# Kernel optimization log

Measured on AMD Instinct MI355X. Metric: run time of the kernel, lower is better.

Reference implementation:

```python
import jax, jax.numpy as jnp
import numpy as np

N, E, G = 50000, 800000, 64
NODE_IN, EDGE_DIM = 128, 16
H1, C1 = 4, 16            # layer1: 4 heads, 16 ch -> concat 64
H2, C2 = 1, 64            # layer2: 1 head, 64 ch, no concat
OUT = 64


def setup_inputs() -> dict:
    key = jax.random.key(0)
    ks = jax.random.split(key, 20)
    s = 0.05
    inp = {
        "x": jax.random.normal(ks[0], (N, NODE_IN), jnp.float32),
        "edge_index": jax.random.randint(ks[1], (2, E), 0, N, jnp.int32),
        "edge_attr": jax.random.normal(ks[2], (E, EDGE_DIM), jnp.float32),
        "batch": jnp.sort(jax.random.randint(ks[3], (N,), 0, G, jnp.int32)),
        # layer 1 params
        "W1": jax.random.normal(ks[4], (NODE_IN, H1 * C1), jnp.float32) * s,
        "as1": jax.random.normal(ks[5], (H1, C1), jnp.float32) * s,
        "ad1": jax.random.normal(ks[6], (H1, C1), jnp.float32) * s,
        "We1": jax.random.normal(ks[7], (EDGE_DIM, H1 * C1), jnp.float32) * s,
        "ae1": jax.random.normal(ks[8], (H1, C1), jnp.float32) * s,
        "b1": jnp.zeros((H1 * C1,), jnp.float32),
        # layer 2 params
        "W2": jax.random.normal(ks[9], (H1 * C1, H2 * C2), jnp.float32) * s,
        "as2": jax.random.normal(ks[10], (H2, C2), jnp.float32) * s,
        "ad2": jax.random.normal(ks[11], (H2, C2), jnp.float32) * s,
        "We2": jax.random.normal(ks[12], (EDGE_DIM, H2 * C2), jnp.float32) * s,
        "ae2": jax.random.normal(ks[13], (H2, C2), jnp.float32) * s,
        "b2": jnp.zeros((C2,), jnp.float32),
        # final projection
        "Pw": jax.random.normal(ks[14], (OUT, OUT), jnp.float32) * s,
        "Pb": jnp.zeros((OUT,), jnp.float32),
    }
    return inp


def _gat(x, src, dst, edge_attr, W, a_s, a_d, We, a_e, b, heads, ch, concat):
    """PyG GATConv: shared lin, edge features, self-loops with mean fill,
    LeakyReLU(0.2), segment softmax over dst, sum aggregation."""
    n = x.shape[0]
    h = (x @ W).reshape(n, heads, ch)                    # [N,H,C]
    al_s = jnp.einsum("nhc,hc->nh", h, a_s)              # [N,H]
    al_d = jnp.einsum("nhc,hc->nh", h, a_d)
    # add self-loops; loop edge_attr = mean of incoming edge attrs (fill='mean')
    deg = jax.ops.segment_sum(jnp.ones((src.shape[0],), x.dtype), dst, n)
    loop_attr = jax.ops.segment_sum(edge_attr, dst, n) / jnp.maximum(deg, 1.0)[:, None]
    ar = jnp.arange(n, dtype=src.dtype)
    s_idx = jnp.concatenate([src, ar])
    d_idx = jnp.concatenate([dst, ar])
    ea = jnp.concatenate([edge_attr, loop_attr], axis=0)
    al_e = jnp.einsum("ehc,hc->eh", (ea @ We).reshape(-1, heads, ch), a_e)
    alpha = jax.nn.leaky_relu(al_s[s_idx] + al_d[d_idx] + al_e, 0.2)  # [E',H]
    # segment softmax over incoming edges of each dst node
    amax = jax.ops.segment_max(alpha, d_idx, num_segments=n)
    ex = jnp.exp(alpha - amax[d_idx])
    denom = jax.ops.segment_sum(ex, d_idx, num_segments=n)
    att = ex / denom[d_idx]                              # safe: self-loops guarantee denom>0
    msg = h[s_idx] * att[..., None]                      # [E',H,C]
    out = jax.ops.segment_sum(msg.reshape(-1, heads * ch), d_idx, num_segments=n)
    out = out if concat else out.reshape(n, heads, ch).mean(axis=1)
    return out + b


def reference(x, edge_index, edge_attr, batch,
              W1, as1, ad1, We1, ae1, b1,
              W2, as2, ad2, We2, ae2, b2, Pw, Pb):
    src, dst = edge_index[0], edge_index[1]
    h = jax.nn.elu(_gat(x, src, dst, edge_attr, W1, as1, ad1, We1, ae1, b1, H1, C1, True))
    h = _gat(h, src, dst, edge_attr, W2, as2, ad2, We2, ae2, b2, H2, C2, False)
    # global mean pool over graphs
    cnt = jax.ops.segment_sum(jnp.ones((N,), h.dtype), batch, num_segments=G)
    pooled = jax.ops.segment_sum(h, batch, num_segments=G) / jnp.maximum(cnt, 1.0)[:, None]
    return pooled @ Pw + Pb
```

## Files before the change

kernel.cpp:

```cpp
#include <hip/hip_runtime.h>

#define LRELU(a) ((a) > 0.f ? (a) : 0.2f * (a))

__device__ __forceinline__ int blockScanIncl256(int v, int* wl) {
  int t = threadIdx.x, lane = t & 63, w = t >> 6;
  int x = v;
#pragma unroll
  for (int o = 1; o < 64; o <<= 1) {
    int tmp = __shfl_up(x, (unsigned)o, 64);
    if (lane >= o) x += tmp;
  }
  if (lane == 63) wl[w] = x;
  __syncthreads();
  if (t == 0) {
    int s = 0;
#pragma unroll
    for (int j = 0; j < 4; ++j) { int tv = wl[j]; wl[j] = s; s += tv; }
  }
  __syncthreads();
  return x + wl[w];
}

__global__ __launch_bounds__(256) void k_deg(const int* __restrict__ dst,
                                             int* __restrict__ deg, int E) {
  int e = blockIdx.x * 256 + threadIdx.x;
  if (e < E) atomicAdd(&deg[dst[e]], 1);
}

__global__ __launch_bounds__(256) void k_chunksum(const int* __restrict__ deg,
                                                  int* __restrict__ bsum, int n) {
  __shared__ int wl[4];
  int i = blockIdx.x * 256 + threadIdx.x;
  int v = (i < n) ? deg[i] : 0;
#pragma unroll
  for (int o = 1; o < 64; o <<= 1) v += __shfl_xor(v, o, 64);
  int lane = threadIdx.x & 63, w = threadIdx.x >> 6;
  if (lane == 0) wl[w] = v;
  __syncthreads();
  if (threadIdx.x == 0) bsum[blockIdx.x] = wl[0] + wl[1] + wl[2] + wl[3];
}

__global__ __launch_bounds__(256) void k_bscan(int* __restrict__ bsum, int nb,
                                               int* __restrict__ csr_off, int n) {
  __shared__ int wl[4];
  int t = threadIdx.x;
  int v = (t < nb) ? bsum[t] : 0;
  int incl = blockScanIncl256(v, wl);
  if (t < nb) bsum[t] = incl - v;
  if (t == 255) csr_off[n] = incl;
}

__global__ __launch_bounds__(256) void k_chunkscan(const int* __restrict__ deg,
                                                   const int* __restrict__ bsum,
                                                   int* __restrict__ csr_off,
                                                   int* __restrict__ fill, int n) {
  __shared__ int wl[4];
  int i = blockIdx.x * 256 + threadIdx.x;
  int v = (i < n) ? deg[i] : 0;
  int incl = blockScanIncl256(v, wl);
  int o = bsum[blockIdx.x] + incl - v;
  if (i < n) { csr_off[i] = o; fill[i] = o; }
}

template <int K, int HH>
__device__ __forceinline__ void gemm_body(const float* __restrict__ X,
                                          const float* __restrict__ W,
                                          const float* __restrict__ a_s,
                                          const float* __restrict__ a_d,
                                          float* __restrict__ H,
                                          float* __restrict__ als,
                                          float* __restrict__ ald,
                                          int n, int bid) {
  constexpr int KC = 32;
  __shared__ float Xs[64][KC + 4];
  __shared__ float Ws[KC][64 + 4];
  int t = threadIdx.x;
  int b0 = bid * 64;
  int tx = t & 15, ty = t >> 4;
  float acc[4][4] = {};
  for (int kc = 0; kc < K; kc += KC) {
    if (kc) __syncthreads();
    {
      int i = t * 8;
      int node = i >> 5, k = i & 31;
      int r = b0 + node;
      float4 v0 = make_float4(0.f, 0.f, 0.f, 0.f), v1 = v0;
      if (r < n) {
        const float* src = X + (size_t)r * K + kc + k;
        v0 = *(const float4*)src;
        v1 = *(const float4*)(src + 4);
      }
      *(float4*)&Xs[node][k] = v0;
      *(float4*)&Xs[node][k + 4] = v1;
    }
    {
      int i = t * 8;
      int kk = i >> 6, c = i & 63;
      const float* src = W + (size_t)(kc + kk) * 64 + c;
      *(float4*)&Ws[kk][c] = *(const float4*)src;
      *(float4*)&Ws[kk][c + 4] = *(const float4*)(src + 4);
    }
    __syncthreads();
#pragma unroll
    for (int k4 = 0; k4 < KC; k4 += 4) {
      float wvf[4][4];
#pragma unroll
      for (int j = 0; j < 4; ++j)
        *(float4*)&wvf[j][0] = *(const float4*)&Ws[k4 + j][tx * 4];
#pragma unroll
      for (int i = 0; i < 4; ++i) {
        float xvf[4];
        *(float4*)&xvf[0] = *(const float4*)&Xs[ty * 4 + i][k4];
#pragma unroll
        for (int kk = 0; kk < 4; ++kk)
#pragma unroll
          for (int j = 0; j < 4; ++j)
            acc[i][j] = fmaf(xvf[kk], wvf[kk][j], acc[i][j]);
      }
    }
  }
#pragma unroll
  for (int i = 0; i < 4; ++i) {
    int node = b0 + ty * 4 + i;
    if (node < n)
      *(float4*)&H[(size_t)node * 64 + tx * 4] =
          make_float4(acc[i][0], acc[i][1], acc[i][2], acc[i][3]);
  }
  constexpr int C = 64 / HH;
  constexpr int GL = C / 4;
  float asv[4], adv[4];
#pragma unroll
  for (int j = 0; j < 4; ++j) { asv[j] = a_s[tx * 4 + j]; adv[j] = a_d[tx * 4 + j]; }
#pragma unroll
  for (int i = 0; i < 4; ++i) {
    float ps = 0.f, pd = 0.f;
#pragma unroll
    for (int j = 0; j < 4; ++j) {
      ps = fmaf(acc[i][j], asv[j], ps);
      pd = fmaf(acc[i][j], adv[j], pd);
    }
#pragma unroll
    for (int o = 1; o < GL; o <<= 1) {
      ps += __shfl_xor(ps, o, 64);
      pd += __shfl_xor(pd, o, 64);
    }
    int node = b0 + ty * 4 + i;
    if (node < n && (tx & (GL - 1)) == 0) {
      int head = tx / GL;
      als[(size_t)node * HH + head] = ps;
      ald[(size_t)node * HH + head] = pd;
    }
  }
}

__global__ __launch_bounds__(256) void k_gemm2(const float* __restrict__ X,
                                               const float* __restrict__ W,
                                               const float* __restrict__ a_s,
                                               const float* __restrict__ a_d,
                                               float* __restrict__ H,
                                               float* __restrict__ als,
                                               float* __restrict__ ald, int n) {
  gemm_body<64, 1>(X, W, a_s, a_d, H, als, ald, n, blockIdx.x);
}

__global__ __launch_bounds__(256) void k_gs(const float* __restrict__ X,
                                            const float* __restrict__ W,
                                            const float* __restrict__ a_s,
                                            const float* __restrict__ a_d,
                                            float* __restrict__ H,
                                            float* __restrict__ als,
                                            float* __restrict__ ald, int n,
                                            int gemmBlocks,
                                            const int* __restrict__ dst,
                                            const int* __restrict__ src,
                                            int* __restrict__ fill,
                                            int2* __restrict__ pack, int E) {
  if ((int)blockIdx.x < gemmBlocks) {
    gemm_body<128, 4>(X, W, a_s, a_d, H, als, ald, n, blockIdx.x);
  } else {
    int base = (blockIdx.x - gemmBlocks) * 512 + threadIdx.x;
    int e0 = base, e1 = base + 256;
    int d0 = 0, d1 = 0;
    if (e0 < E) d0 = dst[e0];
    if (e1 < E) d1 = dst[e1];
    if (e0 < E) {
      int p = atomicAdd(&fill[d0], 1);
      pack[p] = make_int2(e0, src[e0]);
    }
    if (e1 < E) {
      int p = atomicAdd(&fill[d1], 1);
      pack[p] = make_int2(e1, src[e1]);
    }
  }
}

__global__ __launch_bounds__(256) void k_csrlog(
    const int* __restrict__ csr_off, const int2* __restrict__ pack,
    const float* __restrict__ edge_attr,
    const float* __restrict__ We1, const float* __restrict__ ae1,
    const float* __restrict__ We2, const float* __restrict__ ae2,
    const float* __restrict__ als1, const float* __restrict__ ald1,
    float* __restrict__ elog1, float* __restrict__ selfl1,
    float* __restrict__ ed2csr, float* __restrict__ loopdot2, int n) {
  __shared__ float wa1s[64];
  __shared__ float wa2s[16];
  int t = threadIdx.x;
  if (t < 64) {
    int k = t >> 2, hh = t & 3;
    float s = 0.f;
#pragma unroll
    for (int c = 0; c < 16; ++c) s = fmaf(We1[k * 64 + hh * 16 + c], ae1[hh * 16 + c], s);
    wa1s[t] = s;
  } else if (t < 80) {
    int k = t - 64;
    float s = 0.f;
#pragma unroll
    for (int c = 0; c < 64; ++c) s = fmaf(We2[k * 64 + c], ae2[c], s);
    wa2s[k] = s;
  }
  __syncthreads();
  int g = t >> 4, lane16 = t & 15;
  int node = blockIdx.x * 16 + g;
  if (node >= n) return;
  int s0 = csr_off[node], s1 = csr_off[node + 1];
  float4 adv = *(const float4*)(ald1 + (size_t)node * 4);
  float4 sum1 = make_float4(0.f, 0.f, 0.f, 0.f);
  float sum2 = 0.f;
  for (int i = s0 + lane16; i < s1; i += 16) {
    int2 p = pack[i];
    const float4* ea = (const float4*)(edge_attr + (size_t)p.x * 16);
    float ev[16];
    *(float4*)&ev[0]  = ea[0];
    *(float4*)&ev[4]  = ea[1];
    *(float4*)&ev[8]  = ea[2];
    *(float4*)&ev[12] = ea[3];
    float d0 = 0.f, d1 = 0.f, d2 = 0.f, d3 = 0.f, q = 0.f;
#pragma unroll
    for (int k = 0; k < 16; ++k) {
      float4 w1 = *(const float4*)&wa1s[k * 4];
      d0 = fmaf(ev[k], w1.x, d0);
      d1 = fmaf(ev[k], w1.y, d1);
      d2 = fmaf(ev[k], w1.z, d2);
      d3 = fmaf(ev[k], w1.w, d3);
      q  = fmaf(ev[k], wa2s[k], q);
    }
    sum1.x += d0; sum1.y += d1; sum1.z += d2; sum1.w += d3; sum2 += q;
    float4 asv = *(const float4*)(als1 + (size_t)p.y * 4);
    float l0 = asv.x + adv.x + d0;
    float l1 = asv.y + adv.y + d1;
    float l2 = asv.z + adv.z + d2;
    float l3 = asv.w + adv.w + d3;
    *(float4*)&elog1[(size_t)i * 4] =
        make_float4(LRELU(l0), LRELU(l1), LRELU(l2), LRELU(l3));
    ed2csr[i] = q;
  }
#pragma unroll
  for (int o = 1; o < 16; o <<= 1) {
    sum1.x += __shfl_xor(sum1.x, o, 64);
    sum1.y += __shfl_xor(sum1.y, o, 64);
    sum1.z += __shfl_xor(sum1.z, o, 64);
    sum1.w += __shfl_xor(sum1.w, o, 64);
    sum2   += __shfl_xor(sum2,   o, 64);
  }
  if (lane16 == 0) {
    float cd = fmaxf((float)(s1 - s0), 1.f);
    float4 asn = *(const float4*)(als1 + (size_t)node * 4);
    float l0 = asn.x + adv.x + sum1.x / cd;
    float l1 = asn.y + adv.y + sum1.y / cd;
    float l2 = asn.z + adv.z + sum1.z / cd;
    float l3 = asn.w + adv.w + sum1.w / cd;
    *(float4*)&selfl1[(size_t)node * 4] =
        make_float4(LRELU(l0), LRELU(l1), LRELU(l2), LRELU(l3));
    loopdot2[node] = sum2 / cd;
  }
}

__global__ __launch_bounds__(256) void k_agg1(const int* __restrict__ csr_off,
                                              const int2* __restrict__ pack,
                                              const float* __restrict__ elog,
                                              const float* __restrict__ selfl,
                                              const float* __restrict__ h1,
                                              const float* __restrict__ b1,
                                              float* __restrict__ out1, int n) {
  int t = threadIdx.x, w = t >> 6, lane = t & 63;
  int node = blockIdx.x * 4 + w;
  if (node >= n) return;
  int s0 = csr_off[node], s1 = csr_off[node + 1];
  int nit = s1 - s0;
  int h4 = lane & 3;
  float sl4 = selfl[node * 4 + h4];
  float m = sl4;
  for (int i = s0 + (lane >> 2); i < s1; i += 16)
    m = fmaxf(m, elog[(size_t)i * 4 + h4]);
#pragma unroll
  for (int o = 4; o < 64; o <<= 1) m = fmaxf(m, __shfl_xor(m, o, 64));
  float den = ((lane >> 2) == 0) ? __expf(sl4 - m) : 0.f;
  for (int i = s0 + (lane >> 2); i < s1; i += 16)
    den += __expf(elog[(size_t)i * 4 + h4] - m);
#pragma unroll
  for (int o = 4; o < 64; o <<= 1) den += __shfl_xor(den, o, 64);
  int head = lane >> 4;
  float m_ch = __shfl(m, head, 64);
  float rd_ch = 1.f / __shfl(den, head, 64);
  float sl_ch = __shfl(sl4, head, 64);
  float acc = __expf(sl_ch - m_ch) * h1[(size_t)node * 64 + lane];
  if (nit > 0) {
    int nb = (nit + 7) >> 3;
    int laneE = lane & 7, laneB = (lane >> 2) & 7, laneH = lane & 3;
    int sv; float ev;
    float bufA[8], bufB[8];
    {
      int i1 = min(s0 + laneE, s1 - 1);
      sv = pack[i1].y;
      int i2 = min(s0 + laneB, s1 - 1);
      ev = elog[(size_t)i2 * 4 + laneH];
    }
#pragma unroll
    for (int j = 0; j < 8; ++j)
      bufA[j] = h1[(size_t)__shfl(sv, j, 64) * 64 + lane];
    for (int b = 0; b < nb; ++b) {
      int svN = 0; float evN = 0.f;
      bool pf = (b + 1 < nb);
      if (pf) {
        int base = s0 + (b + 1) * 8;
        int i1 = min(base + laneE, s1 - 1);
        svN = pack[i1].y;
        int i2 = min(base + laneB, s1 - 1);
        evN = elog[(size_t)i2 * 4 + laneH];
#pragma unroll
        for (int j = 0; j < 8; ++j)
          bufB[j] = h1[(size_t)__shfl(svN, j, 64) * 64 + lane];
      }
      int rem = nit - b * 8;
#pragma unroll
      for (int j = 0; j < 8; ++j) {
        float aj = __shfl(ev, j * 4 + head, 64);
        float ex = (j < rem) ? __expf(aj - m_ch) : 0.f;
        acc = fmaf(ex, bufA[j], acc);
      }
      if (pf) {
#pragma unroll
        for (int j = 0; j < 8; ++j) bufA[j] = bufB[j];
        sv = svN; ev = evN;
      }
    }
  }
  float r = acc * rd_ch + b1[lane];
  out1[(size_t)node * 64 + lane] = r > 0.f ? r : expm1f(r);
}

__global__ __launch_bounds__(256) void k_l2log(const int* __restrict__ csr_off,
                                               const int2* __restrict__ pack,
                                               const float* __restrict__ eadot2,
                                               const float* __restrict__ loopdot2,
                                               const float* __restrict__ als2,
                                               const float* __restrict__ ald2,
                                               float* __restrict__ elog2,
                                               float* __restrict__ selfl2, int n) {
  int t = threadIdx.x, w = t >> 6, lane = t & 63;
  int node = blockIdx.x * 4 + w;
  if (node >= n) return;
  float adv = ald2[node];
  if (lane == 0) {
    float lg = als2[node] + adv + loopdot2[node];
    selfl2[node] = LRELU(lg);
  }
  int s0 = csr_off[node], s1 = csr_off[node + 1];
  for (int i = s0 + lane; i < s1; i += 64) {
    int s = pack[i].y;
    float lg = als2[s] + adv + eadot2[i];
    elog2[i] = LRELU(lg);
  }
}

__global__ __launch_bounds__(256) void k_agg2(const int* __restrict__ csr_off,
                                              const int2* __restrict__ pack,
                                              const float* __restrict__ elog,
                                              const float* __restrict__ selfl,
                                              const float* __restrict__ h2,
                                              const float* __restrict__ b2,
                                              float* __restrict__ out2, int n) {
  int t = threadIdx.x, w = t >> 6, lane = t & 63;
  int node = blockIdx.x * 4 + w;
  if (node >= n) return;
  int s0 = csr_off[node], s1 = csr_off[node + 1];
  int nit = s1 - s0;
  float sl = selfl[node];
  float m = sl;
  for (int i = s0 + lane; i < s1; i += 64) m = fmaxf(m, elog[i]);
#pragma unroll
  for (int o = 1; o < 64; o <<= 1) m = fmaxf(m, __shfl_xor(m, o, 64));
  float den = (lane == 0) ? __expf(sl - m) : 0.f;
  for (int i = s0 + lane; i < s1; i += 64) den += __expf(elog[i] - m);
#pragma unroll
  for (int o = 1; o < 64; o <<= 1) den += __shfl_xor(den, o, 64);
  float rd = 1.f / den;
  float acc = __expf(sl - m) * h2[(size_t)node * 64 + lane];
  if (nit > 0) {
    int nb = (nit + 7) >> 3;
    int laneE = lane & 7;
    int sv; float ev;
    {
      int i1 = min(s0 + laneE, s1 - 1);
      sv = pack[i1].y;
      ev = elog[i1];
    }
    float bufA[8], bufB[8];
#pragma unroll
    for (int j = 0; j < 8; ++j)
      bufA[j] = h2[(size_t)__shfl(sv, j, 64) * 64 + lane];
    for (int b = 0; b < nb; ++b) {
      int svN = 0; float evN = 0.f;
      bool pf = (b + 1 < nb);
      if (pf) {
        int i1 = min(s0 + (b + 1) * 8 + laneE, s1 - 1);
        svN = pack[i1].y;
        evN = elog[i1];
#pragma unroll
        for (int j = 0; j < 8; ++j)
          bufB[j] = h2[(size_t)__shfl(svN, j, 64) * 64 + lane];
      }
      int rem = nit - b * 8;
#pragma unroll
      for (int j = 0; j < 8; ++j) {
        float aj = __shfl(ev, j, 64);
        float ex = (j < rem) ? __expf(aj - m) : 0.f;
        acc = fmaf(ex, bufA[j], acc);
      }
      if (pf) {
#pragma unroll
        for (int j = 0; j < 8; ++j) bufA[j] = bufB[j];
        sv = svN; ev = evN;
      }
    }
  }
  out2[(size_t)node * 64 + lane] = acc * rd + b2[lane];
}

__global__ __launch_bounds__(256) void k_pool(const float* __restrict__ out2,
                                              const int* __restrict__ batch,
                                              float* __restrict__ pooled,
                                              float* __restrict__ cnt, int n) {
  int wgl = blockIdx.x * 4 + (threadIdx.x >> 6);
  int lane = threadIdx.x & 63;
  int i0 = wgl * 64;
  if (i0 >= n) return;
  int i1 = min(i0 + 64, n);
  int cur = -1;
  float acc = 0.f, c = 0.f;
  for (int i = i0; i < i1; ++i) {
    int g = batch[i];
    if (g != cur) {
      if (cur >= 0) {
        atomicAdd(&pooled[cur * 64 + lane], acc);
        if (lane == 0) atomicAdd(&cnt[cur], c);
      }
      cur = g; acc = 0.f; c = 0.f;
    }
    acc += out2[(size_t)i * 64 + lane];
    c += 1.f;
  }
  if (cur >= 0) {
    atomicAdd(&pooled[cur * 64 + lane], acc);
    if (lane == 0) atomicAdd(&cnt[cur], c);
  }
}

__global__ __launch_bounds__(64) void k_final(const float* __restrict__ pooled,
                                              const float* __restrict__ cnt,
                                              const float* __restrict__ Pw,
                                              const float* __restrict__ Pb,
                                              float* __restrict__ out) {
  __shared__ float m[64];
  int g = blockIdx.x, o = threadIdx.x;
  m[o] = pooled[g * 64 + o] / fmaxf(cnt[g], 1.f);
  __syncthreads();
  float s = Pb[o];
#pragma unroll
  for (int c = 0; c < 64; ++c) s = fmaf(m[c], Pw[c * 64 + o], s);
  out[g * 64 + o] = s;
}

extern "C" void kernel_launch(void* const* d_in, const int* in_sizes, int n_in,
                              void* d_out, int out_size, void* d_ws, size_t ws_size,
                              hipStream_t stream) {
  const float* x         = (const float*)d_in[0];
  const int*   edge_index= (const int*)d_in[1];
  const float* edge_attr = (const float*)d_in[2];
  const int*   batch     = (const int*)d_in[3];
  const float* W1  = (const float*)d_in[4];
  const float* as1 = (const float*)d_in[5];
  const float* ad1 = (const float*)d_in[6];
  const float* We1 = (const float*)d_in[7];
  const float* ae1 = (const float*)d_in[8];
  const float* b1  = (const float*)d_in[9];
  const float* W2  = (const float*)d_in[10];
  const float* as2 = (const float*)d_in[11];
  const float* ad2 = (const float*)d_in[12];
  const float* We2 = (const float*)d_in[13];
  const float* ae2 = (const float*)d_in[14];
  const float* b2  = (const float*)d_in[15];
  const float* Pw  = (const float*)d_in[16];
  const float* Pb  = (const float*)d_in[17];

  const int N = in_sizes[0] / 128;
  const int E = in_sizes[1] / 2;
  const int G = out_size / 64;
  const int* srcI = edge_index;
  const int* dstI = edge_index + E;

  float* ws = (float*)d_ws;
  size_t off = 0;
  auto alloc = [&](size_t elems) {
    float* p = ws + off;
    off += (elems + 3) & ~(size_t)3;
    return p;
  };
  int*   deg       = (int*)alloc(N);
  float* cnt       = alloc(G);
  float* pooled    = alloc((size_t)G * 64);
  size_t zero_bytes = off * sizeof(float);
  int*   csr_off   = (int*)alloc(N + 1);
  int*   fill      = (int*)alloc(N);
  int*   bsum      = (int*)alloc(1024);
  int2*  pack      = (int2*)alloc((size_t)E * 2);
  float* ed2csr    = alloc((size_t)E);
  float* loopdot2  = alloc((size_t)N);
  float* h         = alloc((size_t)N * 64);
  float* als       = alloc((size_t)N * 4);
  float* ald       = alloc((size_t)N * 4);
  float* selfl     = alloc((size_t)N * 4);
  float* elog      = alloc((size_t)E * 4);
  float* outn      = alloc((size_t)N * 64);

  (void)ws_size; (void)n_in;
  hipMemsetAsync(d_ws, 0, zero_bytes, stream);

  const int ebl   = (E + 255) / 256;
  const int nb    = (N + 255) / 256;
  const int nbl4  = (N + 3) / 4;
  const int nbl16 = (N + 15) / 16;
  const int gemb  = (N + 63) / 64;
  const int sctb  = (E + 511) / 512;

  k_deg<<<ebl, 256, 0, stream>>>(dstI, deg, E);
  k_chunksum<<<nb, 256, 0, stream>>>(deg, bsum, N);
  k_bscan<<<1, 256, 0, stream>>>(bsum, nb, csr_off, N);
  k_chunkscan<<<nb, 256, 0, stream>>>(deg, bsum, csr_off, fill, N);

  k_gs<<<gemb + sctb, 256, 0, stream>>>(x, W1, as1, ad1, h, als, ald, N, gemb,
                                        dstI, srcI, fill, pack, E);

  k_csrlog<<<nbl16, 256, 0, stream>>>(csr_off, pack, edge_attr, We1, ae1, We2, ae2,
                                      als, ald, elog, selfl, ed2csr, loopdot2, N);
  k_agg1<<<nbl4, 256, 0, stream>>>(csr_off, pack, elog, selfl, h, b1, outn, N);

  k_gemm2<<<gemb, 256, 0, stream>>>(outn, W2, as2, ad2, h, als, ald, N);
  k_l2log<<<nbl4, 256, 0, stream>>>(csr_off, pack, ed2csr, loopdot2, als, ald,
                                    elog, selfl, N);
  k_agg2<<<nbl4, 256, 0, stream>>>(csr_off, pack, elog, selfl, h, b2, outn, N);

  k_pool<<<((N + 63) / 64 + 3) / 4, 256, 0, stream>>>(outn, batch, pooled, cnt, N);
  k_final<<<G, 64, 0, stream>>>(pooled, cnt, Pw, Pb, (float*)d_out);
}
```

Measured before the change: 287.4 us.

## Fuse edge-attr dots into CSR scatter and compute logits on the fly

Edge-attribute projections for both layers are now computed during the CSR scatter, in coalesced edge order. They are written into a 32-byte packed per-edge record that also holds the source index. This removes the separate k_csrlog and k_l2log kernels and the elog/selfl/ed2csr buffers. The aggregation kernels recompute LeakyReLU logits from the packed record and use an online softmax that merges max and sum into one pass, with self-loop attributes derived from the same loop. The cost is more redundant gathers of als per edge in the aggregation kernels and a wider per-edge record written through atomic-scattered positions.

Result: faster. 244.1 us (-15.0%).

```diff
diff --git a/kernel.cpp b/kernel.cpp
--- a/kernel.cpp
+++ b/kernel.cpp
@@ -173,147 +173,131 @@
                                             int gemmBlocks,
                                             const int* __restrict__ dst,
                                             const int* __restrict__ src,
+                                            const float* __restrict__ edge_attr,
+                                            const float* __restrict__ We1,
+                                            const float* __restrict__ ae1,
+                                            const float* __restrict__ We2,
+                                            const float* __restrict__ ae2,
                                             int* __restrict__ fill,
-                                            int2* __restrict__ pack, int E) {
+                                            float* __restrict__ epk, int E) {
   if ((int)blockIdx.x < gemmBlocks) {
     gemm_body<128, 4>(X, W, a_s, a_d, H, als, ald, n, blockIdx.x);
   } else {
-    int base = (blockIdx.x - gemmBlocks) * 512 + threadIdx.x;
-    int e0 = base, e1 = base + 256;
-    int d0 = 0, d1 = 0;
-    if (e0 < E) d0 = dst[e0];
-    if (e1 < E) d1 = dst[e1];
-    if (e0 < E) {
-      int p = atomicAdd(&fill[d0], 1);
-      pack[p] = make_int2(e0, src[e0]);
-    }
-    if (e1 < E) {
-      int p = atomicAdd(&fill[d1], 1);
-      pack[p] = make_int2(e1, src[e1]);
-    }
-  }
-}
-
-__global__ __launch_bounds__(256) void k_csrlog(
-    const int* __restrict__ csr_off, const int2* __restrict__ pack,
-    const float* __restrict__ edge_attr,
-    const float* __restrict__ We1, const float* __restrict__ ae1,
-    const float* __restrict__ We2, const float* __restrict__ ae2,
-    const float* __restrict__ als1, const float* __restrict__ ald1,
-    float* __restrict__ elog1, float* __restrict__ selfl1,
-    float* __restrict__ ed2csr, float* __restrict__ loopdot2, int n) {
-  __shared__ float wa1s[64];
-  __shared__ float wa2s[16];
-  int t = threadIdx.x;
-  if (t < 64) {
-    int k = t >> 2, hh = t & 3;
-    float s = 0.f;
-#pragma unroll
-    for (int c = 0; c < 16; ++c) s = fmaf(We1[k * 64 + hh * 16 + c], ae1[hh * 16 + c], s);
-    wa1s[t] = s;
-  } else if (t < 80) {
-    int k = t - 64;
-    float s = 0.f;
-#pragma unroll
-    for (int c = 0; c < 64; ++c) s = fmaf(We2[k * 64 + c], ae2[c], s);
-    wa2s[k] = s;
-  }
-  __syncthreads();
-  int g = t >> 4, lane16 = t & 15;
-  int node = blockIdx.x * 16 + g;
-  if (node >= n) return;
-  int s0 = csr_off[node], s1 = csr_off[node + 1];
-  float4 adv = *(const float4*)(ald1 + (size_t)node * 4);
-  float4 sum1 = make_float4(0.f, 0.f, 0.f, 0.f);
-  float sum2 = 0.f;
-  for (int i = s0 + lane16; i < s1; i += 16) {
-    int2 p = pack[i];
-    const float4* ea = (const float4*)(edge_attr + (size_t)p.x * 16);
-    float ev[16];
-    *(float4*)&ev[0]  = ea[0];
-    *(float4*)&ev[4]  = ea[1];
-    *(float4*)&ev[8]  = ea[2];
-    *(float4*)&ev[12] = ea[3];
-    float d0 = 0.f, d1 = 0.f, d2 = 0.f, d3 = 0.f, q = 0.f;
-#pragma unroll
-    for (int k = 0; k < 16; ++k) {
-      float4 w1 = *(const float4*)&wa1s[k * 4];
-      d0 = fmaf(ev[k], w1.x, d0);
-      d1 = fmaf(ev[k], w1.y, d1);
-      d2 = fmaf(ev[k], w1.z, d2);
-      d3 = fmaf(ev[k], w1.w, d3);
-      q  = fmaf(ev[k], wa2s[k], q);
-    }
-    sum1.x += d0; sum1.y += d1; sum1.z += d2; sum1.w += d3; sum2 += q;
-    float4 asv = *(const float4*)(als1 + (size_t)p.y * 4);
-    float l0 = asv.x + adv.x + d0;
-    float l1 = asv.y + adv.y + d1;
-    float l2 = asv.z + adv.z + d2;
-    float l3 = asv.w + adv.w + d3;
-    *(float4*)&elog1[(size_t)i * 4] =
-        make_float4(LRELU(l0), LRELU(l1), LRELU(l2), LRELU(l3));
-    ed2csr[i] = q;
-  }
-#pragma unroll
-  for (int o = 1; o < 16; o <<= 1) {
-    sum1.x += __shfl_xor(sum1.x, o, 64);
-    sum1.y += __shfl_xor(sum1.y, o, 64);
-    sum1.z += __shfl_xor(sum1.z, o, 64);
-    sum1.w += __shfl_xor(sum1.w, o, 64);
-    sum2   += __shfl_xor(sum2,   o, 64);
-  }
-  if (lane16 == 0) {
-    float cd = fmaxf((float)(s1 - s0), 1.f);
-    float4 asn = *(const float4*)(als1 + (size_t)node * 4);
-    float l0 = asn.x + adv.x + sum1.x / cd;
-    float l1 = asn.y + adv.y + sum1.y / cd;
-    float l2 = asn.z + adv.z + sum1.z / cd;
-    float l3 = asn.w + adv.w + sum1.w / cd;
-    *(float4*)&selfl1[(size_t)node * 4] =
-        make_float4(LRELU(l0), LRELU(l1), LRELU(l2), LRELU(l3));
-    loopdot2[node] = sum2 / cd;
+    __shared__ float wa1s[64];
+    __shared__ float wa2s[16];
+    int t = threadIdx.x;
+    if (t < 64) {
+      int k = t >> 2, hh = t & 3;
+      float s = 0.f;
+#pragma unroll
+      for (int c = 0; c < 16; ++c)
+        s = fmaf(We1[k * 64 + hh * 16 + c], ae1[hh * 16 + c], s);
+      wa1s[t] = s;
+    } else if (t < 80) {
+      int k = t - 64;
+      float s = 0.f;
+#pragma unroll
+      for (int c = 0; c < 64; ++c) s = fmaf(We2[k * 64 + c], ae2[c], s);
+      wa2s[k] = s;
+    }
+    __syncthreads();
+    int base = (blockIdx.x - gemmBlocks) * 512 + t;
+#pragma unroll
+    for (int r = 0; r < 2; ++r) {
+      int e = base + r * 256;
+      if (e < E) {
+        int d = dst[e], s = src[e];
+        const float4* ea = (const float4*)(edge_attr + (size_t)e * 16);
+        float ev[16];
+        *(float4*)&ev[0]  = ea[0];
+        *(float4*)&ev[4]  = ea[1];
+        *(float4*)&ev[8]  = ea[2];
+        *(float4*)&ev[12] = ea[3];
+        float d0 = 0.f, d1 = 0.f, d2 = 0.f, d3 = 0.f, q = 0.f;
+#pragma unroll
+        for (int k = 0; k < 16; ++k) {
+          float4 w1 = *(const float4*)&wa1s[k * 4];
+          d0 = fmaf(ev[k], w1.x, d0);
+          d1 = fmaf(ev[k], w1.y, d1);
+          d2 = fmaf(ev[k], w1.z, d2);
+          d3 = fmaf(ev[k], w1.w, d3);
+          q  = fmaf(ev[k], wa2s[k], q);
+        }
+        int p = atomicAdd(&fill[d], 1);
+        float* o = epk + (size_t)p * 8;
+        *(float4*)o = make_float4(d0, d1, d2, d3);
+        *(float4*)(o + 4) = make_float4(q, __int_as_float(s), 0.f, 0.f);
+      }
+    }
   }
 }
 
 __global__ __launch_bounds__(256) void k_agg1(const int* __restrict__ csr_off,
-                                              const int2* __restrict__ pack,
-                                              const float* __restrict__ elog,
-                                              const float* __restrict__ selfl,
+                                              const float* __restrict__ epk,
+                                              const float* __restrict__ als1,
+                                              const float* __restrict__ ald1,
                                               const float* __restrict__ h1,
                                               const float* __restrict__ b1,
-                                              float* __restrict__ out1, int n) {
+                                              float* __restrict__ out1,
+                                              float* __restrict__ loopdot2, int n) {
   int t = threadIdx.x, w = t >> 6, lane = t & 63;
   int node = blockIdx.x * 4 + w;
   if (node >= n) return;
   int s0 = csr_off[node], s1 = csr_off[node + 1];
   int nit = s1 - s0;
-  int h4 = lane & 3;
-  float sl4 = selfl[node * 4 + h4];
-  float m = sl4;
-  for (int i = s0 + (lane >> 2); i < s1; i += 16)
-    m = fmaxf(m, elog[(size_t)i * 4 + h4]);
-#pragma unroll
-  for (int o = 4; o < 64; o <<= 1) m = fmaxf(m, __shfl_xor(m, o, 64));
-  float den = ((lane >> 2) == 0) ? __expf(sl4 - m) : 0.f;
-  for (int i = s0 + (lane >> 2); i < s1; i += 16)
-    den += __expf(elog[(size_t)i * 4 + h4] - m);
-#pragma unroll
-  for (int o = 4; o < 64; o <<= 1) den += __shfl_xor(den, o, 64);
+  int laneB = lane >> 2, laneH = lane & 3;
+  float adv = ald1[(size_t)node * 4 + laneH];
+  float m = -3e38f, den = 0.f, sumd = 0.f, sumq = 0.f;
+  for (int i = s0 + laneB; i < s1; i += 16) {
+    float d = epk[(size_t)i * 8 + laneH];
+    int s = __float_as_int(epk[(size_t)i * 8 + 5]);
+    float q = epk[(size_t)i * 8 + 4];
+    float a = als1[(size_t)s * 4 + laneH] + adv + d;
+    a = LRELU(a);
+    float nm = fmaxf(m, a);
+    den = den * __expf(m - nm) + __expf(a - nm);
+    m = nm;
+    sumd += d;
+    if (laneH == 0) sumq += q;
+  }
+#pragma unroll
+  for (int o = 4; o < 64; o <<= 1) {
+    float om = __shfl_xor(m, o, 64);
+    float od = __shfl_xor(den, o, 64);
+    float nm = fmaxf(m, om);
+    den = den * __expf(m - nm) + od * __expf(om - nm);
+    m = nm;
+    sumd += __shfl_xor(sumd, o, 64);
+    sumq += __shfl_xor(sumq, o, 64);
+  }
+  float cd = fmaxf((float)nit, 1.f);
+  float sl = als1[(size_t)node * 4 + laneH] + adv + sumd / cd;
+  sl = LRELU(sl);
+  {
+    float nm = fmaxf(m, sl);
+    den = den * __expf(m - nm) + __expf(sl - nm);
+    m = nm;
+  }
+  if (lane == 0) loopdot2[node] = sumq / cd;
   int head = lane >> 4;
   float m_ch = __shfl(m, head, 64);
   float rd_ch = 1.f / __shfl(den, head, 64);
-  float sl_ch = __shfl(sl4, head, 64);
+  float sl_ch = __shfl(sl, head, 64);
   float acc = __expf(sl_ch - m_ch) * h1[(size_t)node * 64 + lane];
+  float adv_h = __shfl(adv, head, 64);
   if (nit > 0) {
     int nb = (nit + 7) >> 3;
-    int laneE = lane & 7, laneB = (lane >> 2) & 7, laneH = lane & 3;
+    int laneE = lane & 7, laneB8 = (lane >> 2) & 7;
     int sv; float ev;
     float bufA[8], bufB[8];
     {
       int i1 = min(s0 + laneE, s1 - 1);
-      sv = pack[i1].y;
-      int i2 = min(s0 + laneB, s1 - 1);
-      ev = elog[(size_t)i2 * 4 + laneH];
+      sv = __float_as_int(epk[(size_t)i1 * 8 + 5]);
+      int i2 = min(s0 + laneB8, s1 - 1);
+      float d = epk[(size_t)i2 * 8 + laneH];
+      int se = __float_as_int(epk[(size_t)i2 * 8 + 5]);
+      ev = als1[(size_t)se * 4 + laneH] + adv + d;
+      ev = LRELU(ev);
     }
 #pragma unroll
     for (int j = 0; j < 8; ++j)
@@ -324,9 +308,12 @@
       if (pf) {
         int base = s0 + (b + 1) * 8;
         int i1 = min(base + laneE, s1 - 1);
-        svN = pack[i1].y;
-        int i2 = min(base + laneB, s1 - 1);
-        evN = elog[(size_t)i2 * 4 + laneH];
+        svN = __float_as_int(epk[(size_t)i1 * 8 + 5]);
+        int i2 = min(base + laneB8, s1 - 1);
+        float d = epk[(size_t)i2 * 8 + laneH];
+        int se = __float_as_int(epk[(size_t)i2 * 8 + 5]);
+        evN = als1[(size_t)se * 4 + laneH] + adv + d;
+        evN = LRELU(evN);
 #pragma unroll
         for (int j = 0; j < 8; ++j)
           bufB[j] = h1[(size_t)__shfl(svN, j, 64) * 64 + lane];
@@ -347,36 +334,14 @@
   }
   float r = acc * rd_ch + b1[lane];
   out1[(size_t)node * 64 + lane] = r > 0.f ? r : expm1f(r);
-}
-
-__global__ __launch_bounds__(256) void k_l2log(const int* __restrict__ csr_off,
-                                               const int2* __restrict__ pack,
-                                               const float* __restrict__ eadot2,
-                                               const float* __restrict__ loopdot2,
-                                               const float* __restrict__ als2,
-                                               const float* __restrict__ ald2,
-                                               float* __restrict__ elog2,
-                                               float* __restrict__ selfl2, int n) {
-  int t = threadIdx.x, w = t >> 6, lane = t & 63;
-  int node = blockIdx.x * 4 + w;
-  if (node >= n) return;
-  float adv = ald2[node];
-  if (lane == 0) {
-    float lg = als2[node] + adv + loopdot2[node];
-    selfl2[node] = LRELU(lg);
-  }
-  int s0 = csr_off[node], s1 = csr_off[node + 1];
-  for (int i = s0 + lane; i < s1; i += 64) {
-    int s = pack[i].y;
-    float lg = als2[s] + adv + eadot2[i];
-    elog2[i] = LRELU(lg);
-  }
+  (void)adv_h;
 }
 
 __global__ __launch_bounds__(256) void k_agg2(const int* __restrict__ csr_off,
-                                              const int2* __restrict__ pack,
-                                              const float* __restrict__ elog,
-                                              const float* __restrict__ selfl,
+                                              const float* __restrict__ epk,
+                                              const float* __restrict__ als2,
+                                              const float* __restrict__ ald2,
+                                              const float* __restrict__ loopdot2,
                                               const float* __restrict__ h2,
                                               const float* __restrict__ b2,
                                               float* __restrict__ out2, int n) {
@@ -385,15 +350,32 @@
   if (node >= n) return;
   int s0 = csr_off[node], s1 = csr_off[node + 1];
   int nit = s1 - s0;
-  float sl = selfl[node];
-  float m = sl;
-  for (int i = s0 + lane; i < s1; i += 64) m = fmaxf(m, elog[i]);
-#pragma unroll
-  for (int o = 1; o < 64; o <<= 1) m = fmaxf(m, __shfl_xor(m, o, 64));
-  float den = (lane == 0) ? __expf(sl - m) : 0.f;
-  for (int i = s0 + lane; i < s1; i += 64) den += __expf(elog[i] - m);
-#pragma unroll
-  for (int o = 1; o < 64; o <<= 1) den += __shfl_xor(den, o, 64);
+  float adv = ald2[node];
+  float m = -3e38f, den = 0.f;
+  for (int i = s0 + lane; i < s1; i += 64) {
+    float q = epk[(size_t)i * 8 + 4];
+    int s = __float_as_int(epk[(size_t)i * 8 + 5]);
+    float a = als2[s] + adv + q;
+    a = LRELU(a);
+    float nm = fmaxf(m, a);
+    den = den * __expf(m - nm) + __expf(a - nm);
+    m = nm;
+  }
+#pragma unroll
+  for (int o = 1; o < 64; o <<= 1) {
+    float om = __shfl_xor(m, o, 64);
+    float od = __shfl_xor(den, o, 64);
+    float nm = fmaxf(m, om);
+    den = den * __expf(m - nm) + od * __expf(om - nm);
+    m = nm;
+  }
+  float sl = als2[node] + adv + loopdot2[node];
+  sl = LRELU(sl);
+  {
+    float nm = fmaxf(m, sl);
+    den = den * __expf(m - nm) + __expf(sl - nm);
+    m = nm;
+  }
   float rd = 1.f / den;
   float acc = __expf(sl - m) * h2[(size_t)node * 64 + lane];
   if (nit > 0) {
@@ -402,8 +384,9 @@
     int sv; float ev;
     {
       int i1 = min(s0 + laneE, s1 - 1);
-      sv = pack[i1].y;
-      ev = elog[i1];
+      float q = epk[(size_t)i1 * 8 + 4];
+      sv = __float_as_int(epk[(size_t)i1 * 8 + 5]);
+      ev = LRELU(als2[sv] + adv + q);
     }
     float bufA[8], bufB[8];
 #pragma unroll
@@ -414,8 +397,9 @@
       bool pf = (b + 1 < nb);
       if (pf) {
         int i1 = min(s0 + (b + 1) * 8 + laneE, s1 - 1);
-        svN = pack[i1].y;
-        evN = elog[i1];
+        float q = epk[(size_t)i1 * 8 + 4];
+        svN = __float_as_int(epk[(size_t)i1 * 8 + 5]);
+        evN = LRELU(als2[svN] + adv + q);
 #pragma unroll
         for (int j = 0; j < 8; ++j)
           bufB[j] = h2[(size_t)__shfl(svN, j, 64) * 64 + lane];
@@ -513,7 +497,7 @@
   size_t off = 0;
   auto alloc = [&](size_t elems) {
     float* p = ws + off;
-    off += (elems + 3) & ~(size_t)3;
+    off += (elems + 7) & ~(size_t)7;
     return p;
   };
   int*   deg       = (int*)alloc(N);
@@ -523,14 +507,11 @@
   int*   csr_off   = (int*)alloc(N + 1);
   int*   fill      = (int*)alloc(N);
   int*   bsum      = (int*)alloc(1024);
-  int2*  pack      = (int2*)alloc((size_t)E * 2);
-  float* ed2csr    = alloc((size_t)E);
+  float* epk       = alloc((size_t)E * 8);
   float* loopdot2  = alloc((size_t)N);
   float* h         = alloc((size_t)N * 64);
   float* als       = alloc((size_t)N * 4);
   float* ald       = alloc((size_t)N * 4);
-  float* selfl     = alloc((size_t)N * 4);
-  float* elog      = alloc((size_t)E * 4);
   float* outn      = alloc((size_t)N * 64);
 
   (void)ws_size; (void)n_in;
@@ -539,7 +520,6 @@
   const int ebl   = (E + 255) / 256;
   const int nb    = (N + 255) / 256;
   const int nbl4  = (N + 3) / 4;
-  const int nbl16 = (N + 15) / 16;
   const int gemb  = (N + 63) / 64;
   const int sctb  = (E + 511) / 512;
 
@@ -549,16 +529,13 @@
   k_chunkscan<<<nb, 256, 0, stream>>>(deg, bsum, csr_off, fill, N);
 
   k_gs<<<gemb + sctb, 256, 0, stream>>>(x, W1, as1, ad1, h, als, ald, N, gemb,
-                                        dstI, srcI, fill, pack, E);
-
-  k_csrlog<<<nbl16, 256, 0, stream>>>(csr_off, pack, edge_attr, We1, ae1, We2, ae2,
-                                      als, ald, elog, selfl, ed2csr, loopdot2, N);
-  k_agg1<<<nbl4, 256, 0, stream>>>(csr_off, pack, elog, selfl, h, b1, outn, N);
+                                        dstI, srcI, edge_attr, We1, ae1, We2, ae2,
+                                        fill, epk, E);
+
+  k_agg1<<<nbl4, 256, 0, stream>>>(csr_off, epk, als, ald, h, b1, outn, loopdot2, N);
 
   k_gemm2<<<gemb, 256, 0, stream>>>(outn, W2, as2, ad2, h, als, ald, N);
-  k_l2log<<<nbl4, 256, 0, stream>>>(csr_off, pack, ed2csr, loopdot2, als, ald,
-                                    elog, selfl, N);
-  k_agg2<<<nbl4, 256, 0, stream>>>(csr_off, pack, elog, selfl, h, b2, outn, N);
+  k_agg2<<<nbl4, 256, 0, stream>>>(csr_off, epk, als, ald, loopdot2, h, b2, outn, N);
 
   k_pool<<<((N + 63) / 64 + 3) / 4, 256, 0, stream>>>(outn, batch, pooled, cnt, N);
   k_final<<<G, 64, 0, stream>>>(pooled, cnt, Pw, Pb, (float*)d_out);
```
